# Kernel tuning notes

Hardware: AMD Instinct MI355X
Metric: run time of the kernel (lower is better)

## Reference

```python
import jax, jax.numpy as jnp
from jax import lax
import numpy as np

C_IN, D_INNER, D_STATE, OUT_CH = 20, 32, 8, 20
DT_RANK = max(1, D_INNER // 8)
B, H, W = 4, 384, 384
EPS = 1e-5


def layernorm(x, g, b):
    m = jnp.mean(x, axis=-1, keepdims=True)
    v = jnp.mean((x - m) ** 2, axis=-1, keepdims=True)
    return (x - m) * lax.rsqrt(v + EPS) * g + b


def ss1d(x, xw, dw, db, A_log, Dp):
    # x: (Bb, L, Dd). Mamba selective scan: h_t = exp(dt*A)*h_{t-1} + dt*B_t*u_t; y_t = C_t.h_t + D*u_t
    Bb, L, Dd = x.shape
    N = A_log.shape[1]
    xdbl = x @ xw.T                                   # (Bb, L, dtr+2N)
    dt_lo, Bm, Cm = jnp.split(xdbl, [DT_RANK, DT_RANK + N], axis=-1)
    dt = jax.nn.softplus(dt_lo @ dw.T + db)           # (Bb, L, Dd)
    A = -jnp.exp(A_log)                               # (Dd, N)

    def step(h, inp):
        dt_t, B_t, C_t, u_t = inp                     # (Bb,Dd),(Bb,N),(Bb,N),(Bb,Dd)
        dA = jnp.exp(dt_t[:, :, None] * A)            # (Bb, Dd, N)
        h = dA * h + (dt_t * u_t)[:, :, None] * B_t[:, None, :]
        y = jnp.einsum('bdn,bn->bd', h, C_t)
        return h, y

    xs = (jnp.moveaxis(dt, 1, 0), jnp.moveaxis(Bm, 1, 0),
          jnp.moveaxis(Cm, 1, 0), jnp.moveaxis(x, 1, 0))
    h0 = jnp.zeros((Bb, Dd, N), dtype=x.dtype)
    _, ys = lax.scan(step, h0, xs)
    return jnp.moveaxis(ys, 0, 1) + x * Dp


def setup_inputs() -> dict:
    key = jax.random.key(0)
    ks = jax.random.split(key, 16)
    s = lambda k, shp, sc=0.05: jax.random.normal(k, shp, dtype=jnp.float32) * sc
    A_log1 = jnp.log(jnp.broadcast_to(jnp.arange(1, D_STATE + 1, dtype=jnp.float32), (D_INNER, D_STATE)))
    return {
        'x': jax.random.normal(ks[0], (B, C_IN, H, W), dtype=jnp.float32),
        'norm_g': jnp.ones((C_IN,), jnp.float32),
        'norm_b': jnp.zeros((C_IN,), jnp.float32),
        'inproj_w': s(ks[1], (D_INNER, C_IN), 0.15),
        'dw_w': s(ks[2], (3, 3, 1, D_INNER), 0.2),
        'dw_b': jnp.zeros((D_INNER,), jnp.float32),
        'ssm_xw': s(ks[3], (4, DT_RANK + 2 * D_STATE, D_INNER), 0.1),
        'ssm_dw': s(ks[4], (4, D_INNER, DT_RANK), 0.5),
        'ssm_db': s(ks[5], (4, D_INNER), 0.5) - 3.0,
        'ssm_Alog': jnp.broadcast_to(A_log1, (4, D_INNER, D_STATE)).copy(),
        'ssm_D': jnp.ones((4, D_INNER), jnp.float32),
        'merge_g': jnp.ones((4 * D_INNER,), jnp.float32),
        'merge_b': jnp.zeros((4 * D_INNER,), jnp.float32),
        'merge_w': s(ks[6], (D_INNER, 4 * D_INNER), 0.1),
        'out_w': s(ks[7], (OUT_CH, D_INNER), 0.15),
        'out_b': jnp.zeros((OUT_CH,), jnp.float32),
    }


def reference(x, norm_g, norm_b, inproj_w, dw_w, dw_b, ssm_xw, ssm_dw, ssm_db,
              ssm_Alog, ssm_D, merge_g, merge_b, merge_w, out_w, out_b):
    Bx, C, Hx, Wx = x.shape
    h = jnp.transpose(x, (0, 2, 3, 1))                      # (B,H,W,C)
    h = layernorm(h, norm_g, norm_b)
    h = jax.nn.silu(h @ inproj_w.T)                          # (B,H,W,Dd)
    h = lax.conv_general_dilated(h, dw_w, (1, 1), 'SAME',
                                 dimension_numbers=('NHWC', 'HWIO', 'NHWC'),
                                 feature_group_count=D_INNER) + dw_b
    h = jax.nn.silu(h)                                       # (B,H,W,Dd)

    p = lambda i: (ssm_xw[i], ssm_dw[i], ssm_db[i], ssm_Alog[i], ssm_D[i])

    x_h = h.reshape(Bx * Hx, Wx, D_INNER)
    y_h_fwd = ss1d(x_h, *p(0)).reshape(Bx, Hx, Wx, D_INNER)
    y_h_bwd = ss1d(x_h[:, ::-1], *p(1))[:, ::-1].reshape(Bx, Hx, Wx, D_INNER)

    x_v = jnp.transpose(h, (0, 2, 1, 3)).reshape(Bx * Wx, Hx, D_INNER)
    y_v_fwd = jnp.transpose(ss1d(x_v, *p(2)).reshape(Bx, Wx, Hx, D_INNER), (0, 2, 1, 3))
    y_v_bwd = jnp.transpose(ss1d(x_v[:, ::-1], *p(3))[:, ::-1].reshape(Bx, Wx, Hx, D_INNER), (0, 2, 1, 3))

    y = jnp.concatenate([y_h_fwd, y_h_bwd, y_v_fwd, y_v_bwd], axis=-1)  # (B,H,W,4*Dd)
    y = layernorm(y, merge_g, merge_b)
    y = y @ merge_w.T                                        # (B,H,W,Dd)
    y = y @ out_w.T + out_b                                  # (B,H,W,out_ch)
    return jnp.transpose(y, (0, 3, 1, 2))                    # (B,out_ch,H,W)
```

## Files before the change

### kernel.cpp

```cpp
#include <hip/hip_runtime.h>

typedef unsigned short u16;
typedef unsigned int   u32;
typedef unsigned long long u64;
typedef float f2 __attribute__((ext_vector_type(2)));

#define CIN  20
#define DIN  32
#define BB   4
#define HH   384
#define WW   384
#define HW   147456
#define BHW  589824
#define EPSF 1e-5f
#define GUARD  65536
#define UGUARD 131072

__device__ __forceinline__ float bflo(u32 u) {
    union { u32 v; float f; } x; x.v = u << 16; return x.f;
}
__device__ __forceinline__ float bfhi(u32 u) {
    union { u32 v; float f; } x; x.v = u & 0xffff0000u; return x.f;
}
__device__ __forceinline__ float bf2f(u16 h) {
    union { u32 v; float f; } x; x.v = ((u32)h) << 16; return x.f;
}
__device__ __forceinline__ u16 f2bf(float f) {
    union { float f; u32 u; } v; v.f = f;
    u32 u = v.u;
    return (u16)((u + 0x7FFFu + ((u >> 16) & 1u)) >> 16);
}
__device__ __forceinline__ float silu_f(float a) {
    return a / (1.f + __expf(-a));
}
__device__ __forceinline__ float softplus_f(float z) {
    return (z > 15.f) ? z : __logf(1.f + __expf(z));
}

__global__ void k_prep(const float* __restrict__ ow, const float* __restrict__ mw,
                       const float* __restrict__ mg, const float* __restrict__ mb,
                       const float* __restrict__ ob,
                       float* __restrict__ Wt, float* __restrict__ rsum,
                       float* __restrict__ c0)
{
    __shared__ float mdot[DIN];
    int t = threadIdx.x;
    if (t < DIN) {
        float s = 0.f;
        for (int k = 0; k < 128; ++k) s += mw[t*128 + k] * mb[k];
        mdot[t] = s;
    }
    {
        int k = t;
        for (int o = 0; o < CIN; ++o) {
            float s = 0.f;
            for (int d = 0; d < DIN; ++d) s += ow[o*DIN + d] * mw[d*128 + k];
            Wt[k*CIN + o] = s * mg[k];
        }
    }
    __syncthreads();
    if (t < CIN) {
        float rs = 0.f;
        for (int k = 0; k < 128; ++k) rs += Wt[k*CIN + t];
        rsum[t] = rs;
        float c = ob[t];
        for (int d = 0; d < DIN; ++d) c += ow[t*DIN + d] * mdot[d];
        c0[t] = c;
    }
}

__global__ __launch_bounds__(256) void k_lnproj(
    const float* __restrict__ x, const float* __restrict__ ng,
    const float* __restrict__ nb, const float* __restrict__ ipw,
    u16* __restrict__ h1)
{
    __shared__ __align__(16) f2 w2_s[CIN*16];
    __shared__ float g_s[CIN], b_s[CIN];
    for (int i = threadIdx.x; i < CIN*16; i += 256) {
        int c = i >> 4, j2 = i & 15;
        w2_s[i] = f2{ ipw[(2*j2)*CIN + c], ipw[(2*j2+1)*CIN + c] };
    }
    if (threadIdx.x < CIN) { g_s[threadIdx.x] = ng[threadIdx.x]; b_s[threadIdx.x] = nb[threadIdx.x]; }
    __syncthreads();

    int p = blockIdx.x*256 + threadIdx.x;
    int b = p / HW, rem = p % HW;
    float v[CIN];
    float m = 0.f;
    #pragma unroll
    for (int c = 0; c < CIN; ++c) { v[c] = x[(b*CIN + c)*HW + rem]; m += v[c]; }
    m *= (1.f/CIN);
    float var = 0.f;
    #pragma unroll
    for (int c = 0; c < CIN; ++c) { float d = v[c]-m; var += d*d; }
    var *= (1.f/CIN);
    float rstd = rsqrtf(var + EPSF);
    #pragma unroll
    for (int c = 0; c < CIN; ++c) v[c] = (v[c]-m)*rstd*g_s[c] + b_s[c];

    f2 o2[16];
    #pragma unroll
    for (int j2 = 0; j2 < 16; ++j2) o2[j2] = f2{0.f, 0.f};
    #pragma unroll
    for (int c = 0; c < CIN; ++c) {
        f2 vc = { v[c], v[c] };
        const float4* wr = (const float4*)&w2_s[c*16];
        #pragma unroll
        for (int jq = 0; jq < 8; ++jq) {
            float4 wp = wr[jq];
            o2[2*jq]   = __builtin_elementwise_fma(f2{wp.x, wp.y}, vc, o2[2*jq]);
            o2[2*jq+1] = __builtin_elementwise_fma(f2{wp.z, wp.w}, vc, o2[2*jq+1]);
        }
    }
    u32 pk[16];
    #pragma unroll
    for (int j2 = 0; j2 < 16; ++j2) {
        float a = silu_f(o2[j2].x);
        float c = silu_f(o2[j2].y);
        pk[j2] = (u32)f2bf(a) | ((u32)f2bf(c) << 16);
    }
    uint4* dst = (uint4*)(h1 + (size_t)p*DIN);
    dst[0] = make_uint4(pk[0],pk[1],pk[2],pk[3]);
    dst[1] = make_uint4(pk[4],pk[5],pk[6],pk[7]);
    dst[2] = make_uint4(pk[8],pk[9],pk[10],pk[11]);
    dst[3] = make_uint4(pk[12],pk[13],pk[14],pk[15]);
}

__global__ __launch_bounds__(256) void k_conv(
    const u16* __restrict__ h1, const float* __restrict__ cw,
    const float* __restrict__ cb, u16* __restrict__ h2)
{
    __shared__ __align__(16) f2 w2_s[9*16];
    __shared__ f2 b2_s[16];
    for (int i = threadIdx.x; i < 9*16; i += 256)
        w2_s[i] = f2{ cw[2*i], cw[2*i+1] };
    if (threadIdx.x < 16)
        b2_s[threadIdx.x] = f2{ cb[2*threadIdx.x], cb[2*threadIdx.x+1] };
    __syncthreads();

    int tid = blockIdx.x*256 + threadIdx.x;
    int p = tid >> 2, g = tid & 3;
    int b = p / HW, rem = p % HW;
    int yy0 = rem / WW, xx0 = rem % WW;

    f2 acc2[4];
    #pragma unroll
    for (int i = 0; i < 4; ++i) acc2[i] = b2_s[g*4 + i];

    #pragma unroll
    for (int dy = -1; dy <= 1; ++dy) {
        int yy = yy0 + dy;
        #pragma unroll
        for (int dx = -1; dx <= 1; ++dx) {
            int xc = xx0 + dx;
            if (yy >= 0 && yy < HH && xc >= 0 && xc < WW) {
                uint4 q = *(const uint4*)(h1 + ((size_t)(b*HW + yy*WW + xc)*DIN + g*8));
                int k = (dy+1)*3 + (dx+1);
                const float4* wp4 = (const float4*)&w2_s[k*16 + g*4];
                float4 wA = wp4[0], wB = wp4[1];
                acc2[0] = __builtin_elementwise_fma(f2{wA.x,wA.y}, f2{bflo(q.x),bfhi(q.x)}, acc2[0]);
                acc2[1] = __builtin_elementwise_fma(f2{wA.z,wA.w}, f2{bflo(q.y),bfhi(q.y)}, acc2[1]);
                acc2[2] = __builtin_elementwise_fma(f2{wB.x,wB.y}, f2{bflo(q.z),bfhi(q.z)}, acc2[2]);
                acc2[3] = __builtin_elementwise_fma(f2{wB.z,wB.w}, f2{bflo(q.w),bfhi(q.w)}, acc2[3]);
            }
        }
    }
    u32 pk[4];
    #pragma unroll
    for (int i2 = 0; i2 < 4; ++i2) {
        float a = silu_f(acc2[i2].x);
        float c = silu_f(acc2[i2].y);
        pk[i2] = (u32)f2bf(a) | ((u32)f2bf(c) << 16);
    }
    *(uint4*)(h2 + ((size_t)p*DIN + g*8)) = make_uint4(pk[0],pk[1],pk[2],pk[3]);
}

__global__ __launch_bounds__(256) void k_proj(
    const u16* __restrict__ h2, const float* __restrict__ xw,
    u16* __restrict__ dlA, u16* __restrict__ bcA)
{
    __shared__ __align__(16) f2 xw2_s[4*DIN*10];
    for (int i = threadIdx.x; i < 4*DIN*10; i += 256) {
        int dir = i / 320, r = i % 320;
        int d = r / 10, j2 = r % 10;
        xw2_s[i] = f2{ xw[(dir*CIN + 2*j2)*DIN + d],
                       xw[(dir*CIN + 2*j2 + 1)*DIN + d] };
    }
    __syncthreads();

    int p = blockIdx.x*256 + threadIdx.x;
    float u[DIN];
    const uint4* src = (const uint4*)(h2 + (size_t)p*DIN);
    #pragma unroll
    for (int q4 = 0; q4 < 4; ++q4) {
        uint4 v = src[q4];
        u[q4*8+0]=bflo(v.x); u[q4*8+1]=bfhi(v.x);
        u[q4*8+2]=bflo(v.y); u[q4*8+3]=bfhi(v.y);
        u[q4*8+4]=bflo(v.z); u[q4*8+5]=bfhi(v.z);
        u[q4*8+6]=bflo(v.w); u[q4*8+7]=bfhi(v.w);
    }
    #pragma unroll 1
    for (int dir = 0; dir < 4; ++dir) {
        f2 xd2[10];
        #pragma unroll
        for (int j2 = 0; j2 < 10; ++j2) xd2[j2] = f2{0.f, 0.f};
        #pragma unroll
        for (int d = 0; d < DIN; ++d) {
            f2 ud = { u[d], u[d] };
            const float4* wr = (const float4*)&xw2_s[(dir*DIN + d)*10];
            #pragma unroll
            for (int jq = 0; jq < 5; ++jq) {
                float4 wp = wr[jq];
                xd2[2*jq]   = __builtin_elementwise_fma(f2{wp.x, wp.y}, ud, xd2[2*jq]);
                xd2[2*jq+1] = __builtin_elementwise_fma(f2{wp.z, wp.w}, ud, xd2[2*jq+1]);
            }
        }
        u32 pk[10];
        #pragma unroll
        for (int i = 0; i < 10; ++i)
            pk[i] = (u32)f2bf(xd2[i].x) | ((u32)f2bf(xd2[i].y) << 16);
        *(uint2*)(dlA + (size_t)(dir*BHW + p)*4) = make_uint2(pk[0], pk[1]);
        uint4* bcd = (uint4*)(bcA + (size_t)(dir*BHW + p)*16);
        bcd[0] = make_uint4(pk[2], pk[3], pk[4], pk[5]);
        bcd[1] = make_uint4(pk[6], pk[7], pk[8], pk[9]);
    }
}

__global__ __launch_bounds__(256) void k_scan(
    const char* __restrict__ h2b,
    const char* __restrict__ dlb_,
    const char* __restrict__ bcb_,
    const float* __restrict__ Alog, const float* __restrict__ Dp,
    const float* __restrict__ dwm,  const float* __restrict__ dbv,
    char* __restrict__ y4b)
{
    int tid  = blockIdx.x*256 + threadIdx.x;
    int wv   = tid >> 6, lane = tid & 63;
    int half = lane >> 5, d = lane & 31;
    int dir  = wv / 768;
    int s    = (wv % 768)*2 + half;
    int b    = s / 384, r = s % 384;

    int p0, stp;
    if (dir == 0)      { p0 = b*HW + r*WW;           stp = 1;  }
    else if (dir == 1) { p0 = b*HW + r*WW + (WW-1);  stp = -1; }
    else if (dir == 2) { p0 = b*HW + r;              stp = WW; }
    else               { p0 = b*HW + (HH-1)*WW + r;  stp = -WW;}

    float Av[8];
    bool okl = true;
    #pragma unroll
    for (int j = 0; j < 8; ++j) {
        float e = __expf(Alog[(dir*DIN + d)*8 + j]);
        Av[j] = -e;
        okl = okl && (__builtin_fabsf(e - (float)(j+1)) < 2e-3f);
    }
    bool fast = (__ballot(okl) == ~0ull);

    float Dd  = Dp[dir*DIN + d];
    float dw0 = dwm[(dir*DIN + d)*4 + 0], dw1 = dwm[(dir*DIN + d)*4 + 1];
    float dw2 = dwm[(dir*DIN + d)*4 + 2], dw3 = dwm[(dir*DIN + d)*4 + 3];
    float dbc = dbv[dir*DIN + d];

    u32 uo = UGUARD + (u32)((p0*DIN + d)*2);           int su = stp*DIN*2;
    u32 yo = (u32)((dir*BHW + p0)*64 + d*2);           int sy = stp*64;
    u32 c1 = GUARD + (u32)((dir*BHW + p0)*8);          int s1 = stp*8;
    u32 c2 = GUARD + (u32)((dir*BHW + p0)*32);         int s2 = stp*32;

    u16 ub[4]; uint2 dlr[4]; uint4 B4[4], C4[4];
    u32 fu = uo, f1 = c1, f2o = c2;

    auto fetch = [&](int sl) {
        ub[sl]  = *(const u16*)(h2b + fu);
        dlr[sl] = *(const uint2*)(dlb_ + f1);
        B4[sl]  = *(const uint4*)(bcb_ + f2o);
        C4[sl]  = *(const uint4*)(bcb_ + f2o + 16);
        fu += (u32)su; f1 += (u32)s1; f2o += (u32)s2;
    };

    #pragma unroll
    for (int i = 0; i < 4; ++i) fetch(i);

    f2 h0 = {0.f,0.f}, h1v = {0.f,0.f}, h2v = {0.f,0.f}, h3 = {0.f,0.f};

    if (fast) {
        f2 a01, a23, a45, a67;
        f2 Bq0, Bq1, Bq2, Bq3;
        f2 Cp0, Cp1, Cp2, Cp3;
        float ydc;

        auto prep = [&](int sl) {
            float uu = bf2f(ub[sl]);
            uint2 dl = dlr[sl];
            uint4 Bv = B4[sl], Cv = C4[sl];
            float z = dbc + dw0*bflo(dl.x) + dw1*bfhi(dl.x)
                          + dw2*bflo(dl.y) + dw3*bfhi(dl.y);
            z = fminf(z, 80.f);
            float ez = __expf(z);
            float w  = 1.f + ez;
            float rr = __builtin_amdgcn_rcpf(w);
            float dt = __logf(w);
            float r2 = rr*rr;
            f2 rr2 = {r2, r2};
            f2 t01 = {rr, r2};
            a01 = t01;
            a23 = t01*rr2;
            a45 = a23*rr2;
            a67 = a45*rr2;
            float dtu = dt*uu;
            f2 du2 = {dtu, dtu};
            f2 Bp0 = { bflo(Bv.x), bfhi(Bv.x) }, Bp1 = { bflo(Bv.y), bfhi(Bv.y) };
            f2 Bp2 = { bflo(Bv.z), bfhi(Bv.z) }, Bp3 = { bflo(Bv.w), bfhi(Bv.w) };
            Bq0 = du2*Bp0; Bq1 = du2*Bp1; Bq2 = du2*Bp2; Bq3 = du2*Bp3;
            f2 c0 = { bflo(Cv.x), bfhi(Cv.x) }, c1v = { bflo(Cv.y), bfhi(Cv.y) };
            f2 c2v = { bflo(Cv.z), bfhi(Cv.z) }, c3 = { bflo(Cv.w), bfhi(Cv.w) };
            Cp0 = c0; Cp1 = c1v; Cp2 = c2v; Cp3 = c3;
            ydc = Dd*uu;
        };

        prep(0);

        #pragma unroll 4
        for (int t = 0; t < 384; ++t) {
            int sl = t & 3;
            fetch(sl);

            h0  = __builtin_elementwise_fma(a01, h0,  Bq0);
            h1v = __builtin_elementwise_fma(a23, h1v, Bq1);
            h2v = __builtin_elementwise_fma(a45, h2v, Bq2);
            h3  = __builtin_elementwise_fma(a67, h3,  Bq3);

            f2 yv = Cp0*h0;
            yv = __builtin_elementwise_fma(Cp1, h1v, yv);
            yv = __builtin_elementwise_fma(Cp2, h2v, yv);
            yv = __builtin_elementwise_fma(Cp3, h3,  yv);
            float y = yv.x + yv.y + ydc;

            prep((t+1) & 3);

            *(u16*)(y4b + yo) = f2bf(y);
            yo += (u32)sy;
        }
    } else {
        f2 A2[4];
        #pragma unroll
        for (int j = 0; j < 4; ++j) { A2[j].x = Av[2*j]; A2[j].y = Av[2*j+1]; }
        #pragma unroll 4
        for (int t = 0; t < 384; ++t) {
            int sl = t & 3;
            float uu = bf2f(ub[sl]);
            uint2 dl = dlr[sl];
            uint4 Bv = B4[sl], Cv = C4[sl];
            fetch(sl);

            float z = dbc + dw0*bflo(dl.x) + dw1*bfhi(dl.x)
                          + dw2*bflo(dl.y) + dw3*bfhi(dl.y);
            float dt = softplus_f(z);
            f2 dt2 = {dt, dt};
            f2 e0 = dt2*A2[0], e1 = dt2*A2[1], e2 = dt2*A2[2], e3 = dt2*A2[3];
            f2 a01 = { __expf(e0.x), __expf(e0.y) };
            f2 a23 = { __expf(e1.x), __expf(e1.y) };
            f2 a45 = { __expf(e2.x), __expf(e2.y) };
            f2 a67 = { __expf(e3.x), __expf(e3.y) };

            float dtu = dt*uu;
            f2 du2 = {dtu, dtu};
            f2 Bp0 = { bflo(Bv.x), bfhi(Bv.x) }, Bp1 = { bflo(Bv.y), bfhi(Bv.y) };
            f2 Bp2 = { bflo(Bv.z), bfhi(Bv.z) }, Bp3 = { bflo(Bv.w), bfhi(Bv.w) };
            f2 Cp0 = { bflo(Cv.x), bfhi(Cv.x) }, Cp1 = { bflo(Cv.y), bfhi(Cv.y) };
            f2 Cp2 = { bflo(Cv.z), bfhi(Cv.z) }, Cp3 = { bflo(Cv.w), bfhi(Cv.w) };

            h0  = __builtin_elementwise_fma(a01, h0,  du2*Bp0);
            h1v = __builtin_elementwise_fma(a23, h1v, du2*Bp1);
            h2v = __builtin_elementwise_fma(a45, h2v, du2*Bp2);
            h3  = __builtin_elementwise_fma(a67, h3,  du2*Bp3);

            f2 yv = Cp0*h0;
            yv = __builtin_elementwise_fma(Cp1, h1v, yv);
            yv = __builtin_elementwise_fma(Cp2, h2v, yv);
            yv = __builtin_elementwise_fma(Cp3, h3,  yv);

            float y = yv.x + yv.y + Dd*uu;
            *(u16*)(y4b + yo) = f2bf(y);
            yo += (u32)sy;
        }
    }
}

__global__ __launch_bounds__(256) void k_merge(
    const u16* __restrict__ y4, const float* __restrict__ Wt,
    const float* __restrict__ rsum, const float* __restrict__ c0,
    float* __restrict__ out)
{
    __shared__ __align__(16) f2 Wt2_s[128*10];
    __shared__ float rs_s[CIN], c0_s[CIN];
    for (int i = threadIdx.x; i < 128*10; i += 256) {
        int k = i / 10, o2 = i % 10;
        Wt2_s[i] = f2{ Wt[k*CIN + 2*o2], Wt[k*CIN + 2*o2 + 1] };
    }
    if (threadIdx.x < CIN) { rs_s[threadIdx.x] = rsum[threadIdx.x]; c0_s[threadIdx.x] = c0[threadIdx.x]; }
    __syncthreads();

    int p = blockIdx.x*256 + threadIdx.x;
    int b = p / HW, rem = p % HW;

    float s1 = 0.f, s2 = 0.f;
    f2 acc2[10];
    #pragma unroll
    for (int o2 = 0; o2 < 10; ++o2) acc2[o2] = f2{0.f, 0.f};

    #pragma unroll 1
    for (int dirk = 0; dirk < 4; ++dirk) {
        const uint4* src = (const uint4*)(y4 + ((size_t)dirk*BHW + p)*32);
        #pragma unroll
        for (int q4 = 0; q4 < 4; ++q4) {
            uint4 v = src[q4];
            u32 w[4] = {v.x, v.y, v.z, v.w};
            #pragma unroll
            for (int i = 0; i < 4; ++i) {
                int k = dirk*32 + q4*8 + i*2;
                float a = bflo(w[i]); float c = bfhi(w[i]);
                s1 += a + c; s2 += a*a + c*c;
                f2 af = {a, a}, cf = {c, c};
                const float4* w0 = (const float4*)&Wt2_s[k*10];
                const float4* w1 = (const float4*)&Wt2_s[(k+1)*10];
                #pragma unroll
                for (int jq = 0; jq < 5; ++jq) {
                    float4 x0 = w0[jq], x1 = w1[jq];
                    acc2[2*jq]   = __builtin_elementwise_fma(f2{x0.x, x0.y}, af, acc2[2*jq]);
                    acc2[2*jq]   = __builtin_elementwise_fma(f2{x1.x, x1.y}, cf, acc2[2*jq]);
                    acc2[2*jq+1] = __builtin_elementwise_fma(f2{x0.z, x0.w}, af, acc2[2*jq+1]);
                    acc2[2*jq+1] = __builtin_elementwise_fma(f2{x1.z, x1.w}, cf, acc2[2*jq+1]);
                }
            }
        }
    }
    float m = s1*(1.f/128.f);
    float var = s2*(1.f/128.f) - m*m;
    float rstd = rsqrtf(var + EPSF);
    #pragma unroll
    for (int o2 = 0; o2 < 10; ++o2) {
        float r0 = rstd*(acc2[o2].x - m*rs_s[2*o2])   + c0_s[2*o2];
        float r1 = rstd*(acc2[o2].y - m*rs_s[2*o2+1]) + c0_s[2*o2+1];
        out[(b*CIN + 2*o2)*HW + rem]   = r0;
        out[(b*CIN + 2*o2+1)*HW + rem] = r1;
    }
}

extern "C" void kernel_launch(void* const* d_in, const int* in_sizes, int n_in,
                              void* d_out, int out_size, void* d_ws, size_t ws_size,
                              hipStream_t stream)
{
    const float* x    = (const float*)d_in[0];
    const float* ng   = (const float*)d_in[1];
    const float* nb   = (const float*)d_in[2];
    const float* ipw  = (const float*)d_in[3];
    const float* cw   = (const float*)d_in[4];
    const float* cb   = (const float*)d_in[5];
    const float* xw   = (const float*)d_in[6];
    const float* dwm  = (const float*)d_in[7];
    const float* dbv  = (const float*)d_in[8];
    const float* Alog = (const float*)d_in[9];
    const float* Dpv  = (const float*)d_in[10];
    const float* mg   = (const float*)d_in[11];
    const float* mb   = (const float*)d_in[12];
    const float* mw   = (const float*)d_in[13];
    const float* ow   = (const float*)d_in[14];
    const float* ob   = (const float*)d_in[15];
    float* out = (float*)d_out;

    const size_t y4_bytes = (size_t)4*BHW*DIN*2;
    const size_t dl_bytes = (size_t)4*BHW*8;
    const size_t bc_bytes = (size_t)4*BHW*32;
    const size_t wt_bytes = (size_t)(128*CIN + 64)*4;

    char* ws = (char*)d_ws;
    u16* y4 = (u16*)ws;
    u16* h1 = y4;

    size_t dl_pos = y4_bytes + GUARD;
    size_t bc_pos = dl_pos + dl_bytes + GUARD;
    size_t wt_pos = bc_pos + bc_bytes + GUARD;
    size_t need   = wt_pos + wt_bytes + GUARD;

    if (ws_size < need) {
        hipMemsetAsync(d_out, 0x7F, (size_t)out_size*4, stream);
        return;
    }

    char* h2base = (char*)d_out;
    u16*  h2 = (u16*)(h2base + UGUARD);

    u16* dlA = (u16*)(ws + dl_pos);
    u16* bcA = (u16*)(ws + bc_pos);
    float* Wt   = (float*)(ws + wt_pos);
    float* rsum = Wt + 128*CIN;
    float* c0   = rsum + 32;

    k_prep  <<<1, 128, 0, stream>>>(ow, mw, mg, mb, ob, Wt, rsum, c0);
    k_lnproj<<<BHW/256, 256, 0, stream>>>(x, ng, nb, ipw, h1);
    k_conv  <<<BHW*4/256, 256, 0, stream>>>(h1, cw, cb, h2);
    k_proj  <<<BHW/256, 256, 0, stream>>>(h2, xw, dlA, bcA);
    k_scan  <<<768, 256, 0, stream>>>(
        h2base, (const char*)(ws + dl_pos - GUARD), (const char*)(ws + bc_pos - GUARD),
        Alog, Dpv, dwm, dbv, (char*)y4);
    k_merge <<<BHW/256, 256, 0, stream>>>(y4, Wt, rsum, c0, out);
}
```

Measured before the change: 478.4 us.

## Fuse layernorm/in-projection, depthwise conv and x-projection into one tiled kernel

Replaces three separate kernels (LN+inproj, 3x3 depthwise conv, per-direction x projection) with one kernel working on 16x16 spatial tiles. Each block computes LN+inproj+SiLU for an 18x18 halo region into fp32 shared memory, then runs the conv and projection from there, writing only h2, dl and bc. This drops the global round trip of the intermediate h1 and two launches. In exchange it recomputes the halo (about 27% extra front work), uses about 47KB of shared memory per block, which may limit occupancy, and keeps the intermediate in fp32 rather than bf16, so results change slightly.

```diff
diff --git a/kernel.cpp b/kernel.cpp
--- a/kernel.cpp
+++ b/kernel.cpp
@@ -69,118 +69,35 @@
     }
 }
 
-__global__ __launch_bounds__(256) void k_lnproj(
+#define TS   16
+#define HT   18
+#define CPAD 36
+__global__ __launch_bounds__(256) void k_front(
     const float* __restrict__ x, const float* __restrict__ ng,
     const float* __restrict__ nb, const float* __restrict__ ipw,
-    u16* __restrict__ h1)
+    const float* __restrict__ cw, const float* __restrict__ cb,
+    const float* __restrict__ xw,
+    u16* __restrict__ h2, u16* __restrict__ dlA, u16* __restrict__ bcA)
 {
-    __shared__ __align__(16) f2 w2_s[CIN*16];
+    __shared__ __align__(16) float hs[HT*HT*CPAD];
+    __shared__ __align__(16) f2 wln_s[CIN*16];
     __shared__ float g_s[CIN], b_s[CIN];
-    for (int i = threadIdx.x; i < CIN*16; i += 256) {
+    __shared__ __align__(16) f2 wc_s[9*16];
+    __shared__ __align__(16) f2 bc2_s[16];
+    __shared__ __align__(16) f2 xw2_s[4*DIN*10];
+
+    int tid = threadIdx.x;
+    for (int i = tid; i < CIN*16; i += 256) {
         int c = i >> 4, j2 = i & 15;
-        w2_s[i] = f2{ ipw[(2*j2)*CIN + c], ipw[(2*j2+1)*CIN + c] };
-    }
-    if (threadIdx.x < CIN) { g_s[threadIdx.x] = ng[threadIdx.x]; b_s[threadIdx.x] = nb[threadIdx.x]; }
-    __syncthreads();
-
-    int p = blockIdx.x*256 + threadIdx.x;
-    int b = p / HW, rem = p % HW;
-    float v[CIN];
-    float m = 0.f;
-    #pragma unroll
-    for (int c = 0; c < CIN; ++c) { v[c] = x[(b*CIN + c)*HW + rem]; m += v[c]; }
-    m *= (1.f/CIN);
-    float var = 0.f;
-    #pragma unroll
-    for (int c = 0; c < CIN; ++c) { float d = v[c]-m; var += d*d; }
-    var *= (1.f/CIN);
-    float rstd = rsqrtf(var + EPSF);
-    #pragma unroll
-    for (int c = 0; c < CIN; ++c) v[c] = (v[c]-m)*rstd*g_s[c] + b_s[c];
-
-    f2 o2[16];
-    #pragma unroll
-    for (int j2 = 0; j2 < 16; ++j2) o2[j2] = f2{0.f, 0.f};
-    #pragma unroll
-    for (int c = 0; c < CIN; ++c) {
-        f2 vc = { v[c], v[c] };
-        const float4* wr = (const float4*)&w2_s[c*16];
-        #pragma unroll
-        for (int jq = 0; jq < 8; ++jq) {
-            float4 wp = wr[jq];
-            o2[2*jq]   = __builtin_elementwise_fma(f2{wp.x, wp.y}, vc, o2[2*jq]);
-            o2[2*jq+1] = __builtin_elementwise_fma(f2{wp.z, wp.w}, vc, o2[2*jq+1]);
-        }
-    }
-    u32 pk[16];
-    #pragma unroll
-    for (int j2 = 0; j2 < 16; ++j2) {
-        float a = silu_f(o2[j2].x);
-        float c = silu_f(o2[j2].y);
-        pk[j2] = (u32)f2bf(a) | ((u32)f2bf(c) << 16);
-    }
-    uint4* dst = (uint4*)(h1 + (size_t)p*DIN);
-    dst[0] = make_uint4(pk[0],pk[1],pk[2],pk[3]);
-    dst[1] = make_uint4(pk[4],pk[5],pk[6],pk[7]);
-    dst[2] = make_uint4(pk[8],pk[9],pk[10],pk[11]);
-    dst[3] = make_uint4(pk[12],pk[13],pk[14],pk[15]);
-}
-
-__global__ __launch_bounds__(256) void k_conv(
-    const u16* __restrict__ h1, const float* __restrict__ cw,
-    const float* __restrict__ cb, u16* __restrict__ h2)
-{
-    __shared__ __align__(16) f2 w2_s[9*16];
-    __shared__ f2 b2_s[16];
-    for (int i = threadIdx.x; i < 9*16; i += 256)
-        w2_s[i] = f2{ cw[2*i], cw[2*i+1] };
-    if (threadIdx.x < 16)
-        b2_s[threadIdx.x] = f2{ cb[2*threadIdx.x], cb[2*threadIdx.x+1] };
-    __syncthreads();
-
-    int tid = blockIdx.x*256 + threadIdx.x;
-    int p = tid >> 2, g = tid & 3;
-    int b = p / HW, rem = p % HW;
-    int yy0 = rem / WW, xx0 = rem % WW;
-
-    f2 acc2[4];
-    #pragma unroll
-    for (int i = 0; i < 4; ++i) acc2[i] = b2_s[g*4 + i];
-
-    #pragma unroll
-    for (int dy = -1; dy <= 1; ++dy) {
-        int yy = yy0 + dy;
-        #pragma unroll
-        for (int dx = -1; dx <= 1; ++dx) {
-            int xc = xx0 + dx;
-            if (yy >= 0 && yy < HH && xc >= 0 && xc < WW) {
-                uint4 q = *(const uint4*)(h1 + ((size_t)(b*HW + yy*WW + xc)*DIN + g*8));
-                int k = (dy+1)*3 + (dx+1);
-                const float4* wp4 = (const float4*)&w2_s[k*16 + g*4];
-                float4 wA = wp4[0], wB = wp4[1];
-                acc2[0] = __builtin_elementwise_fma(f2{wA.x,wA.y}, f2{bflo(q.x),bfhi(q.x)}, acc2[0]);
-                acc2[1] = __builtin_elementwise_fma(f2{wA.z,wA.w}, f2{bflo(q.y),bfhi(q.y)}, acc2[1]);
-                acc2[2] = __builtin_elementwise_fma(f2{wB.x,wB.y}, f2{bflo(q.z),bfhi(q.z)}, acc2[2]);
-                acc2[3] = __builtin_elementwise_fma(f2{wB.z,wB.w}, f2{bflo(q.w),bfhi(q.w)}, acc2[3]);
-            }
-        }
-    }
-    u32 pk[4];
-    #pragma unroll
-    for (int i2 = 0; i2 < 4; ++i2) {
-        float a = silu_f(acc2[i2].x);
-        float c = silu_f(acc2[i2].y);
-        pk[i2] = (u32)f2bf(a) | ((u32)f2bf(c) << 16);
-    }
-    *(uint4*)(h2 + ((size_t)p*DIN + g*8)) = make_uint4(pk[0],pk[1],pk[2],pk[3]);
-}
-
-__global__ __launch_bounds__(256) void k_proj(
-    const u16* __restrict__ h2, const float* __restrict__ xw,
-    u16* __restrict__ dlA, u16* __restrict__ bcA)
-{
-    __shared__ __align__(16) f2 xw2_s[4*DIN*10];
-    for (int i = threadIdx.x; i < 4*DIN*10; i += 256) {
+        wln_s[i] = f2{ ipw[(2*j2)*CIN + c], ipw[(2*j2+1)*CIN + c] };
+    }
+    if (tid < CIN) { g_s[tid] = ng[tid]; b_s[tid] = nb[tid]; }
+    if (tid < 144) wc_s[tid] = f2{ cw[2*tid], cw[2*tid+1] };
+    if (tid >= 144 && tid < 160) {
+        int i = tid - 144;
+        bc2_s[i] = f2{ cb[2*i], cb[2*i+1] };
+    }
+    for (int i = tid; i < 4*DIN*10; i += 256) {
         int dir = i / 320, r = i % 320;
         int d = r / 10, j2 = r % 10;
         xw2_s[i] = f2{ xw[(dir*CIN + 2*j2)*DIN + d],
@@ -188,17 +105,97 @@
     }
     __syncthreads();
 
-    int p = blockIdx.x*256 + threadIdx.x;
+    int bx = blockIdx.x;
+    int b  = bx / 576, t6 = bx % 576;
+    int ty0 = (t6 / 24)*TS, tx0 = (t6 % 24)*TS;
+
+    for (int j = tid; j < HT*HT; j += 256) {
+        int hy = j / HT, hx = j % HT;
+        int gy = ty0 + hy - 1, gx = tx0 + hx - 1;
+        float* hp = &hs[(hy*HT + hx)*CPAD];
+        if (gy >= 0 && gy < HH && gx >= 0 && gx < WW) {
+            int rem = gy*WW + gx;
+            float v[CIN];
+            float m = 0.f;
+            #pragma unroll
+            for (int c = 0; c < CIN; ++c) { v[c] = x[(b*CIN + c)*HW + rem]; m += v[c]; }
+            m *= (1.f/CIN);
+            float var = 0.f;
+            #pragma unroll
+            for (int c = 0; c < CIN; ++c) { float d = v[c]-m; var += d*d; }
+            var *= (1.f/CIN);
+            float rstd = rsqrtf(var + EPSF);
+            #pragma unroll
+            for (int c = 0; c < CIN; ++c) v[c] = (v[c]-m)*rstd*g_s[c] + b_s[c];
+
+            f2 o2[16];
+            #pragma unroll
+            for (int j2 = 0; j2 < 16; ++j2) o2[j2] = f2{0.f, 0.f};
+            #pragma unroll
+            for (int c = 0; c < CIN; ++c) {
+                f2 vc = { v[c], v[c] };
+                const float4* wr = (const float4*)&wln_s[c*16];
+                #pragma unroll
+                for (int jq = 0; jq < 8; ++jq) {
+                    float4 wp = wr[jq];
+                    o2[2*jq]   = __builtin_elementwise_fma(f2{wp.x, wp.y}, vc, o2[2*jq]);
+                    o2[2*jq+1] = __builtin_elementwise_fma(f2{wp.z, wp.w}, vc, o2[2*jq+1]);
+                }
+            }
+            #pragma unroll
+            for (int q = 0; q < 8; ++q) {
+                float a0 = silu_f(o2[2*q].x),   a1 = silu_f(o2[2*q].y);
+                float a2 = silu_f(o2[2*q+1].x), a3 = silu_f(o2[2*q+1].y);
+                *(float4*)&hp[4*q] = make_float4(a0, a1, a2, a3);
+            }
+        } else {
+            #pragma unroll
+            for (int q = 0; q < 8; ++q)
+                *(float4*)&hp[4*q] = make_float4(0.f, 0.f, 0.f, 0.f);
+        }
+    }
+    __syncthreads();
+
+    int ty = tid >> 4, tx = tid & 15;
+    int gy = ty0 + ty, gx = tx0 + tx;
+    int p  = b*HW + gy*WW + gx;
+
+    f2 acc2[16];
+    #pragma unroll
+    for (int i = 0; i < 16; ++i) acc2[i] = bc2_s[i];
+
+    #pragma unroll
+    for (int k = 0; k < 9; ++k) {
+        int dy = k/3, dx = k%3;
+        const float* np = &hs[((ty+dy)*HT + (tx+dx))*CPAD];
+        const f2* wk = &wc_s[k*16];
+        #pragma unroll
+        for (int q = 0; q < 8; ++q) {
+            float4 t4 = *(const float4*)&np[4*q];
+            acc2[2*q]   = __builtin_elementwise_fma(wk[2*q],   f2{t4.x, t4.y}, acc2[2*q]);
+            acc2[2*q+1] = __builtin_elementwise_fma(wk[2*q+1], f2{t4.z, t4.w}, acc2[2*q+1]);
+        }
+    }
+
     float u[DIN];
-    const uint4* src = (const uint4*)(h2 + (size_t)p*DIN);
-    #pragma unroll
-    for (int q4 = 0; q4 < 4; ++q4) {
-        uint4 v = src[q4];
-        u[q4*8+0]=bflo(v.x); u[q4*8+1]=bfhi(v.x);
-        u[q4*8+2]=bflo(v.y); u[q4*8+3]=bfhi(v.y);
-        u[q4*8+4]=bflo(v.z); u[q4*8+5]=bfhi(v.z);
-        u[q4*8+6]=bflo(v.w); u[q4*8+7]=bfhi(v.w);
-    }
+    #pragma unroll
+    for (int i = 0; i < 16; ++i) {
+        u[2*i]   = silu_f(acc2[i].x);
+        u[2*i+1] = silu_f(acc2[i].y);
+    }
+
+    {
+        u32 pk[16];
+        #pragma unroll
+        for (int i = 0; i < 16; ++i)
+            pk[i] = (u32)f2bf(u[2*i]) | ((u32)f2bf(u[2*i+1]) << 16);
+        uint4* dst = (uint4*)(h2 + (size_t)p*DIN);
+        dst[0] = make_uint4(pk[0],pk[1],pk[2],pk[3]);
+        dst[1] = make_uint4(pk[4],pk[5],pk[6],pk[7]);
+        dst[2] = make_uint4(pk[8],pk[9],pk[10],pk[11]);
+        dst[3] = make_uint4(pk[12],pk[13],pk[14],pk[15]);
+    }
+
     #pragma unroll 1
     for (int dir = 0; dir < 4; ++dir) {
         f2 xd2[10];
@@ -476,7 +473,6 @@
 
     char* ws = (char*)d_ws;
     u16* y4 = (u16*)ws;
-    u16* h1 = y4;
 
     size_t dl_pos = y4_bytes + GUARD;
     size_t bc_pos = dl_pos + dl_bytes + GUARD;
@@ -498,9 +494,7 @@
     float* c0   = rsum + 32;
 
     k_prep  <<<1, 128, 0, stream>>>(ow, mw, mg, mb, ob, Wt, rsum, c0);
-    k_lnproj<<<BHW/256, 256, 0, stream>>>(x, ng, nb, ipw, h1);
-    k_conv  <<<BHW*4/256, 256, 0, stream>>>(h1, cw, cb, h2);
-    k_proj  <<<BHW/256, 256, 0, stream>>>(h2, xw, dlA, bcA);
+    k_front <<<2304, 256, 0, stream>>>(x, ng, nb, ipw, cw, cb, xw, h2, dlA, bcA);
     k_scan  <<<768, 256, 0, stream>>>(
         h2base, (const char*)(ws + dl_pos - GUARD), (const char*)(ws + bc_pos - GUARD),
         Alog, Dpv, dwm, dbv, (char*)y4);
```

Measured after the change: 765.2 us. +59.9%, slower.
